# Optimization experiments

Hardware: AMD Instinct MI355X
Metric: run time of the kernel (lower is better)

Reference implementation:

```python
import jax, jax.numpy as jnp
import numpy as np
from jax import lax

B, S, D = 8, 96, 768
R, RSEQ, TAG = 24, 8, 3


def setup_inputs() -> dict:
    key = jax.random.key(0)
    k0, k1, k2, k3 = jax.random.split(key, 4)
    encoded_text = jax.random.normal(k0, (B, S, D), jnp.float32)
    rel_types_encoded = jax.random.normal(k1, (R, RSEQ, D), jnp.float32)
    proj_W = jax.random.normal(k2, (2 * D, 3 * D), jnp.float32) * 0.02
    proj_b = jnp.zeros((3 * D,), jnp.float32)
    rel_W = jax.random.normal(k3, (3 * D, R * TAG), jnp.float32) * 0.02
    rel_b = jnp.zeros((R * TAG,), jnp.float32)
    return {
        "encoded_text": encoded_text,
        "rel_types_encoded": rel_types_encoded,
        "proj_W": proj_W,
        "proj_b": proj_b,
        "rel_W": rel_W,
        "rel_b": rel_b,
    }


def _refine(enc, rel_types):
    """Faithful vectorized version of the nested python loops in
    get_encoded_text: for each sample i, R sequential cross-attention
    updates on matrix_b using matrix_a = rel_types_encoded[i] (the
    original code indexes with i, reusing the same matrix_a each step).
    enc: [Bsz, S, D]; rel_types: [R, RSEQ, D].
    """
    Bsz = enc.shape[0]
    d = enc.shape[-1]
    scale = 1.0 / jnp.sqrt(jnp.asarray(d, enc.dtype))
    num_steps = rel_types.shape[0]  # loop runs rel_types_encoded.size(0) times
    A_batch = rel_types[:Bsz]  # matrix_a = rel_types_encoded[i]

    def per_sample(b0, A):  # b0: [S, D], A: [RSEQ, D]
        def step(b, _):
            scores = (A @ b.T) * scale            # [RSEQ, S]
            w = jax.nn.softmax(scores, axis=-1)    # softmax over seq
            return b + w.T @ A, None               # matrix_b += matrix_c
        bf, _ = lax.scan(step, b0, None, length=num_steps)
        return bf

    return jax.vmap(per_sample)(enc, A_batch)


def reference(encoded_text, rel_types_encoded, proj_W, proj_b, rel_W, rel_b):
    enc = _refine(encoded_text, rel_types_encoded)  # [B, S, D]
    Bsz, seq, d = enc.shape
    rel_num = rel_types_encoded.shape[0]
    tag_size = rel_W.shape[1] // rel_num

    # projection(cat(head, tail)) == head @ Wh + tail @ Wt + b; avoid
    # materializing the [B, S*S, 2D] concat (same math as the original).
    Wh, Wt = proj_W[:d], proj_W[d:]
    Hh = enc @ Wh                                   # [B, S, 3D] head part
    Ht = enc @ Wt                                   # [B, S, 3D] tail part
    pairs = Hh[:, :, None, :] + Ht[:, None, :, :] + proj_b  # [B, S, S, 3D]
    pairs = jax.nn.relu(pairs)
    triple = pairs.reshape(Bsz, seq * seq, 3 * d) @ rel_W + rel_b
    triple = triple.reshape(Bsz, seq, seq, rel_num, tag_size)
    return jnp.transpose(triple, (0, 4, 3, 1, 2))  # [B, tag, rel, S, S]
```

## Files before the change

kernel.cpp:

```cpp
#include <hip/hip_runtime.h>
#include <hip/hip_bf16.h>
#include <math.h>
#include <stdint.h>
#include <string.h>

#define BB 8
#define SS 96
#define DD 768
#define RR 24
#define RSEQ 8
#define TAG 3
#define D3 2304
#define NC 72

typedef __attribute__((ext_vector_type(8))) short bf16x8;
typedef __attribute__((ext_vector_type(4))) float f32x4;
typedef _Float16 f16x8 __attribute__((ext_vector_type(8)));
typedef _Float16 f16x2 __attribute__((ext_vector_type(2)));

typedef __attribute__((address_space(3))) uint8_t lds_u8;
typedef const __attribute__((address_space(1))) uint8_t glb_u8;
static __device__ __forceinline__ void glld16(const void* g, void* l) {
  __builtin_amdgcn_global_load_lds((glb_u8*)g, (lds_u8*)l, 16, 0, 0);
}

#define VMW(N) asm volatile("s_waitcnt vmcnt(" #N ")" ::: "memory")

static __device__ inline uint32_t pkrhu(float lo, float hi) {
  uint32_t a, b;
  memcpy(&a, &lo, 4);
  memcpy(&b, &hi, 4);
  return __builtin_amdgcn_perm(b + 0x8000u, a + 0x8000u, 0x07060302u);
}
static __device__ inline uint32_t pkrne(float lo, float hi) {
  uint32_t a, b;
  memcpy(&a, &lo, 4);
  memcpy(&b, &hi, 4);
  a += 0x7FFFu + ((a >> 16) & 1u);
  b += 0x7FFFu + ((b >> 16) & 1u);
  return (a >> 16) | (b & 0xFFFF0000u);
}
static __device__ inline uint32_t pkf16(float lo, float hi) {
  union { f16x2 h; uint32_t u; } r;
  r.h[0] = (_Float16)lo;
  r.h[1] = (_Float16)hi;
  return r.u;
}
static __device__ inline uint16_t f16b(float v) {
  union { _Float16 h; uint16_t u; } r;
  r.h = (_Float16)v;
  return r.u;
}

__global__ __launch_bounds__(256) void k_prep0(const float* __restrict__ relW,
                                               uint16_t* __restrict__ Wb,
                                               const float* __restrict__ projW,
                                               uint16_t* __restrict__ Tp,
                                               const float* __restrict__ enc,
                                               const float* __restrict__ rel,
                                               float* __restrict__ SG) {
  __shared__ __align__(16) char smem[24704];
  const int blk = blockIdx.x;
  const int t = threadIdx.x;

  if (blk < 36) {
    float* tile = (float*)smem;
    const int k0 = blk * 64;
    const float* src = relW + (size_t)k0 * NC;
    for (int e = t; e < 64 * NC / 4; e += 256) ((float4*)tile)[e] = ((const float4*)src)[e];
    __syncthreads();
    for (int u = t; u < 80 * 16; u += 256) {
      const int n = u >> 4, kq = (u & 15) * 4;
      uint2 w = {0u, 0u};
      if (n < NC) {
        w.x = pkf16(tile[(kq + 0) * NC + n], tile[(kq + 1) * NC + n]);
        w.y = pkf16(tile[(kq + 2) * NC + n], tile[(kq + 3) * NC + n]);
      }
      *(uint2*)&Wb[(size_t)n * D3 + k0 + kq] = w;
    }
  } else if (blk < 900) {
    const int bx = blk - 36;
    float (*tile)[65] = (float(*)[65])smem;
    const int c0 = (bx % 36) * 64;
    const int r0 = (bx / 36) * 64;
    {
      const int tr = t >> 4;
      const int tc4 = (t & 15) * 4;
#pragma unroll
      for (int p = 0; p < 4; ++p) {
        const int r = tr + p * 16;
        const float4 v = *(const float4*)&projW[(size_t)(r0 + r) * D3 + c0 + tc4];
        tile[r][tc4 + 0] = v.x;
        tile[r][tc4 + 1] = v.y;
        tile[r][tc4 + 2] = v.z;
        tile[r][tc4 + 3] = v.w;
      }
    }
    __syncthreads();
    {
      const int cc = t >> 4;
      const int rr4 = (t & 15) * 4;
#pragma unroll
      for (int p = 0; p < 4; ++p) {
        const int c = cc + p * 16;
        uint2 w;
        w.x = pkrne(tile[rr4 + 0][c], tile[rr4 + 1][c]);
        w.y = pkrne(tile[rr4 + 2][c], tile[rr4 + 3][c]);
        *(uint2*)&Tp[(size_t)(c0 + c) * (2 * DD) + r0 + rr4] = w;
      }
    }
  } else {
    const int idx = blk - 900;
    const int b = idx >> 4;
    const int d0 = (idx & 15) * 48;
    float (*AsF)[48] = (float(*)[48])smem;

    if (t < 96) {
      const int r = t / 12, q4 = (t % 12) * 4;
      *(float4*)&AsF[r][q4] = *(const float4*)&rel[((size_t)b * RSEQ + r) * DD + d0 + q4];
    }
    __syncthreads();

    for (int e = t; e < RSEQ * (SS + RSEQ); e += 256) {
      const int r = e & 7, s = e >> 3;
      const float* row = (s < SS) ? (enc + ((size_t)b * SS + s) * DD + d0) : &AsF[s - SS][0];
      float a0 = 0.f, a1 = 0.f, a2 = 0.f, a3 = 0.f;
#pragma unroll
      for (int d = 0; d < 48; d += 4) {
        const float4 rv = *(const float4*)&row[d];
        a0 += AsF[r][d + 0] * rv.x;
        a1 += AsF[r][d + 1] * rv.y;
        a2 += AsF[r][d + 2] * rv.z;
        a3 += AsF[r][d + 3] * rv.w;
      }
      atomicAdd(&SG[((size_t)b * RSEQ + r) * 104 + s], (a0 + a1) + (a2 + a3));
    }
  }
}

__global__ __launch_bounds__(256) void k_refS(const float* __restrict__ SG,
                                              float* __restrict__ Pst) {
  const int b = blockIdx.x;
  const int t = threadIdx.x;
  __shared__ float S0[RSEQ][SS];
  __shared__ float G[RSEQ][RSEQ];
  __shared__ float P[RSEQ][SS];
  __shared__ float sc[RSEQ][SS];
  const float scale = 0.036084391824351613f;

  for (int e = t; e < RSEQ * 104; e += 256) {
    const int r = e / 104, c = e % 104;
    const float v = SG[(size_t)b * RSEQ * 104 + e];
    if (c < SS) S0[r][c] = v;
    else G[r][c - SS] = v;
  }
  for (int e = t; e < RSEQ * SS; e += 256) ((float*)P)[e] = 0.f;
  __syncthreads();

  const int wave = t >> 6, lane = t & 63;
  for (int step = 0; step < RR; ++step) {
    for (int e = t; e < RSEQ * SS; e += 256) {
      const int r = e / SS, s = e % SS;
      float acc = S0[r][s];
#pragma unroll
      for (int r2 = 0; r2 < RSEQ; ++r2) acc += G[r][r2] * P[r2][s];
      sc[r][s] = acc * scale;
    }
    __syncthreads();
#pragma unroll
    for (int rr = 0; rr < 2; ++rr) {
      const int r = wave * 2 + rr;
      const float m1 = sc[r][lane];
      const float m2 = (lane < 32) ? sc[r][lane + 64] : -1e30f;
      float mx = fmaxf(m1, m2);
#pragma unroll
      for (int o = 32; o > 0; o >>= 1) mx = fmaxf(mx, __shfl_xor(mx, o, 64));
      const float e1 = __expf(m1 - mx);
      const float e2 = (lane < 32) ? __expf(m2 - mx) : 0.f;
      float sm = e1 + e2;
#pragma unroll
      for (int o = 32; o > 0; o >>= 1) sm += __shfl_xor(sm, o, 64);
      const float inv = 1.f / sm;
      P[r][lane] += e1 * inv;
      if (lane < 32) P[r][lane + 64] += e2 * inv;
    }
    __syncthreads();
  }

  for (int e = t; e < RSEQ * SS; e += 256) Pst[(size_t)b * RSEQ * SS + e] = ((float*)P)[e];
}

__global__ __launch_bounds__(256) void k_refB(const float* __restrict__ enc,
                                              const float* __restrict__ rel,
                                              const float* __restrict__ Pst,
                                              uint16_t* __restrict__ encRb) {
  const int blk = blockIdx.x;
  const int b = blk / 12;
  const int s0 = (blk % 12) * 8;
  const int t = threadIdx.x;
  __shared__ float As[RSEQ][DD + 4];
  __shared__ float Pl[RSEQ][8];

  const float* Ag = rel + (size_t)b * RSEQ * DD;
  for (int e = t; e < RSEQ * DD / 4; e += 256) {
    const int r = (e * 4) / DD, d = (e * 4) % DD;
    *(float4*)&As[r][d] = *(const float4*)&Ag[e * 4];
  }
  if (t < RSEQ * 8) {
    const int r = t >> 3, sl = t & 7;
    Pl[r][sl] = Pst[(size_t)b * RSEQ * SS + r * SS + s0 + sl];
  }
  __syncthreads();

  const float* Eb = enc + ((size_t)b * SS + s0) * DD;
  uint16_t* Ob = encRb + ((size_t)b * SS + s0) * DD;
  for (int e = t; e < 8 * DD / 4; e += 256) {
    const int sl = (e * 4) / DD, d = (e * 4) % DD;
    float4 v = ((const float4*)Eb)[e];
#pragma unroll
    for (int r = 0; r < RSEQ; ++r) {
      const float p = Pl[r][sl];
      v.x += p * As[r][d + 0];
      v.y += p * As[r][d + 1];
      v.z += p * As[r][d + 2];
      v.w += p * As[r][d + 3];
    }
    uint2 w;
    w.x = pkrhu(v.x, v.y);
    w.y = pkrhu(v.z, v.w);
    *(uint2*)&Ob[e * 4] = w;
  }
}

__global__ __launch_bounds__(256, 4) void k_proj(const uint16_t* __restrict__ Ab,
                                                 const uint16_t* __restrict__ Bt,
                                                 const float* __restrict__ pb,
                                                 uint16_t* __restrict__ Hh16,
                                                 uint16_t* __restrict__ Htf) {
  const int m0 = blockIdx.x * 64;
  const int gn0 = blockIdx.y * 64;
  const bool isH = gn0 < D3;
  const int n0 = isH ? gn0 : gn0 - D3;
  const int halfk = isH ? 0 : DD;
  const int t = threadIdx.x, w = t >> 6, lane = t & 63;
  const int wm = w >> 1, wn = w & 1;
  const int lm = lane & 15, q = lane >> 4;

  __shared__ __align__(16) uint16_t As[64 * 72];
  __shared__ __align__(16) uint16_t Bs[64 * 72];

  const char* rp[5];
  char* lp[5];
#pragma unroll
  for (int r = 0; r < 5; ++r) {
    const int idx = w + 4 * r;
    rp[r] = nullptr;
    lp[r] = nullptr;
    if (idx < 18) {
      const int ii = (idx < 9) ? idx : idx - 9;
      const int beta = ii * 1024 + lane * 16;
      const int elem = beta >> 1;
      const int row = elem / 72;
      int o = elem - row * 72;
      if (o >= 64) o = 0;
      if (idx < 9) {
        rp[r] = (const char*)(Ab + (size_t)(m0 + row) * DD + o);
        lp[r] = (char*)As + ii * 1024;
      } else {
        rp[r] = (const char*)(Bt + (size_t)(n0 + row) * (2 * DD) + halfk + o);
        lp[r] = (char*)Bs + ii * 1024;
      }
    }
  }

  f32x4 acc[2][2];
#pragma unroll
  for (int a = 0; a < 2; ++a)
#pragma unroll
    for (int c = 0; c < 2; ++c) acc[a][c] = (f32x4){0.f, 0.f, 0.f, 0.f};

  for (int k0 = 0; k0 < DD; k0 += 64) {
    __syncthreads();
#pragma unroll
    for (int r = 0; r < 5; ++r)
      if (rp[r]) glld16(rp[r] + 2 * k0, lp[r]);
    __syncthreads();
#pragma unroll
    for (int kk = 0; kk < 2; ++kk) {
      const int ko = kk * 32 + q * 8;
      bf16x8 af[2], bf[2];
#pragma unroll
      for (int mt = 0; mt < 2; ++mt)
        af[mt] = *(const bf16x8*)&As[(wm * 32 + mt * 16 + lm) * 72 + ko];
#pragma unroll
      for (int nt = 0; nt < 2; ++nt)
        bf[nt] = *(const bf16x8*)&Bs[(wn * 32 + nt * 16 + lm) * 72 + ko];
#pragma unroll
      for (int nt = 0; nt < 2; ++nt)
#pragma unroll
        for (int mt = 0; mt < 2; ++mt)
          acc[mt][nt] = __builtin_amdgcn_mfma_f32_16x16x32_bf16(af[mt], bf[nt], acc[mt][nt], 0, 0, 0);
    }
  }

#pragma unroll
  for (int nt = 0; nt < 2; ++nt) {
    const int ncol = n0 + wn * 32 + nt * 16 + lm;
    const int mrow = m0 + wm * 32 + q * 4;
    uint16_t* dst = isH ? Hh16 : Htf;
    const float bias = isH ? pb[ncol] : 0.f;
#pragma unroll
    for (int mt = 0; mt < 2; ++mt)
#pragma unroll
      for (int r = 0; r < 4; ++r)
        dst[(size_t)(mrow + mt * 16 + r) * D3 + ncol] = f16b(acc[mt][nt][r] + bias);
  }
}

#define HT_LDS 12288
#define CH_B 22528
#define NISS 22
#define NKC 36
#define NPH 18

__global__ __launch_bounds__(768, 1) void k_pairs(const uint16_t* __restrict__ Hh,
                                                  const uint16_t* __restrict__ Htb,
                                                  const uint16_t* __restrict__ Wb,
                                                  const float* __restrict__ relb,
                                                  float* __restrict__ out) {
  const int blk = blockIdx.x;
  const int b = blk >> 5, ii = blk & 31;
  const int t = threadIdx.x;
  const int w = t >> 6, lane = t & 63;
  const int lm = lane & 15, q = lane >> 4;
  const int iw = w >> 2;
  const int jh = (w >> 1) & 1;
  const int nh = w & 1;
  const int ntn = nh ? 2 : 3;
  const int i = ii * 3 + iw;

  __shared__ __align__(16) uint16_t Hr[7680];
  __shared__ __align__(16) uint16_t Stg[3][CH_B];

  {
    const char* hh = (const char*)(Hh + ((size_t)b * SS + ii * 3) * D3);
#pragma unroll
    for (int r = 0; r < 2; ++r) {
      const int idx = w + 12 * r;
      if (idx < 14) glld16(hh + idx * 1024 + lane * 16, (char*)Hr + idx * 1024);
    }
  }

  const char* rp[2];
#pragma unroll
  for (int r = 0; r < 2; ++r) {
    const int idx = w + 12 * r;
    rp[r] = nullptr;
    if (idx < NISS) {
      const int beta = idx * 1024 + lane * 16;
      if (beta < HT_LDS) {
        const int row = beta >> 7;
        const int real = (beta & 127) ^ ((row & 7) << 4);
        rp[r] = (const char*)(Htb + ((size_t)b * SS + row) * D3 + (real >> 1));
      } else {
        const int bb = beta - HT_LDS;
        const int row = bb >> 7;
        const int real = (bb & 127) ^ ((row & 7) << 4);
        rp[r] = (const char*)(Wb + (size_t)row * D3 + (real >> 1));
      }
    }
  }

#pragma unroll
  for (int pp = 0; pp < 2; ++pp)
#pragma unroll
    for (int kc = 0; kc < 2; ++kc)
#pragma unroll
      for (int r = 0; r < 2; ++r)
        if (rp[r])
          glld16(rp[r] + (size_t)128 * (2 * pp + kc),
                 (char*)Stg[pp] + kc * CH_B + (w + 12 * r) * 1024);

  f32x4 acc[3][3];
#pragma unroll
  for (int mt = 0; mt < 3; ++mt)
#pragma unroll
    for (int nt = 0; nt < 3; ++nt) acc[mt][nt] = (f32x4){0.f, 0.f, 0.f, 0.f};

  const f16x8 zro = {0, 0, 0, 0, 0, 0, 0, 0};

  for (int p = 0; p < NPH; ++p) {
    if (w < 10) VMW(4); else VMW(2);
    __builtin_amdgcn_s_barrier();
    __builtin_amdgcn_sched_barrier(0);

    {
      char* dst = (char*)Stg[(p + 2) % 3];
      int pn = p + 2;
      if (pn >= NPH) pn -= NPH;
#pragma unroll
      for (int kc = 0; kc < 2; ++kc)
#pragma unroll
        for (int r = 0; r < 2; ++r)
          if (rp[r])
            glld16(rp[r] + (size_t)128 * (2 * pn + kc),
                   dst + kc * CH_B + (w + 12 * r) * 1024);
    }

    const char* Sp = (const char*)Stg[p % 3];
#pragma unroll
    for (int kc = 0; kc < 2; ++kc) {
      const char* S = Sp + kc * CH_B;
      const int k0 = (2 * p + kc) * 64;
#pragma unroll
      for (int kk = 0; kk < 2; ++kk) {
        const int ko = kk * 32 + q * 8;
        const int xb = (ko * 2) ^ ((lane & 7) << 4);
        const f16x8 hv = *(const f16x8*)&Hr[iw * D3 + k0 + ko];
        f16x8 af[3];
#pragma unroll
        for (int mt = 0; mt < 3; ++mt) {
          const f16x8 s = *(const f16x8*)(S + (jh * 48 + mt * 16 + lm) * 128 + xb) + hv;
          af[mt] = __builtin_elementwise_max(s, zro);
        }
        f16x8 bfv[3];
#pragma unroll
        for (int nt = 0; nt < 3; ++nt)
          if (nt < ntn)
            bfv[nt] = *(const f16x8*)(S + HT_LDS + (nh * 48 + nt * 16 + lm) * 128 + xb);
        __builtin_amdgcn_s_setprio(1);
#pragma unroll
        for (int nt = 0; nt < 3; ++nt)
          if (nt < ntn)
#pragma unroll
            for (int mt = 0; mt < 3; ++mt)
              acc[mt][nt] = __builtin_amdgcn_mfma_f32_16x16x32_f16(af[mt], bfv[nt], acc[mt][nt], 0, 0, 0);
        __builtin_amdgcn_s_setprio(0);
      }
    }
    asm volatile("s_waitcnt lgkmcnt(0)" ::: "memory");
    __builtin_amdgcn_sched_barrier(0);
  }

  VMW(0);

#pragma unroll
  for (int nt = 0; nt < 3; ++nt) {
    if (nt < ntn) {
      const int c = nh * 48 + nt * 16 + lm;
      if (c < NC) {
        const float rb = relb[c];
        const int rr = c / 3, tg = c % 3;
#pragma unroll
        for (int mt = 0; mt < 3; ++mt) {
          const int j0 = jh * 48 + mt * 16 + q * 4;
          float* base = out + ((((size_t)b * TAG + tg) * RR + rr) * SS + i) * SS + j0;
          float4 o;
          o.x = acc[mt][nt][0] + rb;
          o.y = acc[mt][nt][1] + rb;
          o.z = acc[mt][nt][2] + rb;
          o.w = acc[mt][nt][3] + rb;
          *(float4*)base = o;
        }
      }
    }
  }
}

extern "C" void kernel_launch(void* const* d_in, const int* in_sizes, int n_in,
                              void* d_out, int out_size, void* d_ws, size_t ws_size,
                              hipStream_t stream) {
  const float* enc   = (const float*)d_in[0];
  const float* rel   = (const float*)d_in[1];
  const float* projW = (const float*)d_in[2];
  const float* projb = (const float*)d_in[3];
  const float* relW  = (const float*)d_in[4];
  const float* relb  = (const float*)d_in[5];
  float* out = (float*)d_out;

  uint16_t* Hh16 = (uint16_t*)d_ws;
  uint16_t* Htf  = Hh16 + (size_t)DD * D3 + 512;
  uint16_t* Wb   = Htf + (size_t)DD * D3;
  uint16_t* Tp   = Wb + (size_t)96 * D3;
  uint16_t* Ab   = Tp + (size_t)D3 * 2 * DD;
  float* Pst = (float*)(Ab + (size_t)DD * DD);
  float* SG = Pst + (size_t)BB * RSEQ * SS;

  hipMemsetAsync(SG, 0, (size_t)BB * RSEQ * 104 * sizeof(float), stream);
  k_prep0<<<1028, 256, 0, stream>>>(relW, Wb, projW, Tp, enc, rel, SG);
  k_refS<<<BB, 256, 0, stream>>>(SG, Pst);
  k_refB<<<96, 256, 0, stream>>>(enc, rel, Pst, Ab);
  k_proj<<<dim3(12, 72), 256, 0, stream>>>(Ab, Tp, projb, Hh16, Htf);
  k_pairs<<<256, 768, 0, stream>>>(Hh16, Htf, Wb, relb, out);
}
```

Baseline: 187.8 us.

## Split K across wave pairs instead of N in pairs kernel, reduce via LDS

After: 182.1 us. -3.1%, faster.

```diff
diff --git a/kernel.cpp b/kernel.cpp
--- a/kernel.cpp
+++ b/kernel.cpp
@@ -335,8 +335,7 @@
   const int lm = lane & 15, q = lane >> 4;
   const int iw = w >> 2;
   const int jh = (w >> 1) & 1;
-  const int nh = w & 1;
-  const int ntn = nh ? 2 : 3;
+  const int kh = w & 1;
   const int i = ii * 3 + iw;
 
   __shared__ __align__(16) uint16_t Hr[7680];
@@ -381,11 +380,11 @@
           glld16(rp[r] + (size_t)128 * (2 * pp + kc),
                  (char*)Stg[pp] + kc * CH_B + (w + 12 * r) * 1024);
 
-  f32x4 acc[3][3];
+  f32x4 acc[3][5];
 #pragma unroll
   for (int mt = 0; mt < 3; ++mt)
 #pragma unroll
-    for (int nt = 0; nt < 3; ++nt) acc[mt][nt] = (f32x4){0.f, 0.f, 0.f, 0.f};
+    for (int nt = 0; nt < 5; ++nt) acc[mt][nt] = (f32x4){0.f, 0.f, 0.f, 0.f};
 
   const f16x8 zro = {0, 0, 0, 0, 0, 0, 0, 0};
 
@@ -407,59 +406,62 @@
                    dst + kc * CH_B + (w + 12 * r) * 1024);
     }
 
-    const char* Sp = (const char*)Stg[p % 3];
-#pragma unroll
-    for (int kc = 0; kc < 2; ++kc) {
-      const char* S = Sp + kc * CH_B;
-      const int k0 = (2 * p + kc) * 64;
-#pragma unroll
-      for (int kk = 0; kk < 2; ++kk) {
-        const int ko = kk * 32 + q * 8;
-        const int xb = (ko * 2) ^ ((lane & 7) << 4);
-        const f16x8 hv = *(const f16x8*)&Hr[iw * D3 + k0 + ko];
-        f16x8 af[3];
-#pragma unroll
-        for (int mt = 0; mt < 3; ++mt) {
-          const f16x8 s = *(const f16x8*)(S + (jh * 48 + mt * 16 + lm) * 128 + xb) + hv;
-          af[mt] = __builtin_elementwise_max(s, zro);
-        }
-        f16x8 bfv[3];
-#pragma unroll
-        for (int nt = 0; nt < 3; ++nt)
-          if (nt < ntn)
-            bfv[nt] = *(const f16x8*)(S + HT_LDS + (nh * 48 + nt * 16 + lm) * 128 + xb);
-        __builtin_amdgcn_s_setprio(1);
-#pragma unroll
-        for (int nt = 0; nt < 3; ++nt)
-          if (nt < ntn)
-#pragma unroll
-            for (int mt = 0; mt < 3; ++mt)
-              acc[mt][nt] = __builtin_amdgcn_mfma_f32_16x16x32_f16(af[mt], bfv[nt], acc[mt][nt], 0, 0, 0);
-        __builtin_amdgcn_s_setprio(0);
-      }
+    const char* S = (const char*)Stg[p % 3] + kh * CH_B;
+    const int k0 = (2 * p + kh) * 64;
+#pragma unroll
+    for (int kk = 0; kk < 2; ++kk) {
+      const int ko = kk * 32 + q * 8;
+      const int xb = (ko * 2) ^ ((lane & 7) << 4);
+      const f16x8 hv = *(const f16x8*)&Hr[iw * D3 + k0 + ko];
+      f16x8 af[3];
+#pragma unroll
+      for (int mt = 0; mt < 3; ++mt) {
+        const f16x8 s = *(const f16x8*)(S + (jh * 48 + mt * 16 + lm) * 128 + xb) + hv;
+        af[mt] = __builtin_elementwise_max(s, zro);
+      }
+      f16x8 bfv[5];
+#pragma unroll
+      for (int nt = 0; nt < 5; ++nt)
+        bfv[nt] = *(const f16x8*)(S + HT_LDS + (nt * 16 + lm) * 128 + xb);
+      __builtin_amdgcn_s_setprio(1);
+#pragma unroll
+      for (int nt = 0; nt < 5; ++nt)
+#pragma unroll
+        for (int mt = 0; mt < 3; ++mt)
+          acc[mt][nt] = __builtin_amdgcn_mfma_f32_16x16x32_f16(af[mt], bfv[nt], acc[mt][nt], 0, 0, 0);
+      __builtin_amdgcn_s_setprio(0);
     }
     asm volatile("s_waitcnt lgkmcnt(0)" ::: "memory");
     __builtin_amdgcn_sched_barrier(0);
   }
 
-  VMW(0);
-
-#pragma unroll
-  for (int nt = 0; nt < 3; ++nt) {
-    if (nt < ntn) {
-      const int c = nh * 48 + nt * 16 + lm;
+  __syncthreads();
+  float* RED = (float*)&Stg[0][0];
+  if (w & 1) {
+#pragma unroll
+    for (int mt = 0; mt < 3; ++mt)
+#pragma unroll
+      for (int nt = 0; nt < 5; ++nt)
+        *(f32x4*)&RED[(((w >> 1) * 15 + mt * 5 + nt) << 8) + lane * 4] = acc[mt][nt];
+  }
+  __syncthreads();
+  if (!(w & 1)) {
+#pragma unroll
+    for (int nt = 0; nt < 5; ++nt) {
+      const int c = nt * 16 + lm;
       if (c < NC) {
         const float rb = relb[c];
         const int rr = c / 3, tg = c % 3;
 #pragma unroll
         for (int mt = 0; mt < 3; ++mt) {
+          const f32x4 oth = *(const f32x4*)&RED[(((w >> 1) * 15 + mt * 5 + nt) << 8) + lane * 4];
           const int j0 = jh * 48 + mt * 16 + q * 4;
           float* base = out + ((((size_t)b * TAG + tg) * RR + rr) * SS + i) * SS + j0;
           float4 o;
-          o.x = acc[mt][nt][0] + rb;
-          o.y = acc[mt][nt][1] + rb;
-          o.z = acc[mt][nt][2] + rb;
-          o.w = acc[mt][nt][3] + rb;
+          o.x = acc[mt][nt][0] + oth[0] + rb;
+          o.y = acc[mt][nt][1] + oth[1] + rb;
+          o.z = acc[mt][nt][2] + oth[2] + rb;
+          o.w = acc[mt][nt][3] + oth[3] + rb;
           *(float4*)base = o;
         }
       }
```
